# Optimization experiments

Hardware: AMD Instinct MI355X
Metric: run time of the kernel (lower is better)

The kernel has to match this reference:

```python
import jax, jax.numpy as jnp
import numpy as np

IN_DIM, HIDDEN_DIM, OUT_DIM = 128, 256, 128
N_NODES, N_EDGES = 100000, 1000000


def setup_inputs() -> dict:
    key = jax.random.key(0)
    ks = jax.random.split(key, 8)
    s = lambda d: 1.0 / np.sqrt(d)
    x = jax.random.normal(ks[0], (N_NODES, IN_DIM), dtype=jnp.float32)
    edge_index = jax.random.randint(ks[1], (2, N_EDGES), 0, N_NODES, dtype=jnp.int64)
    # encoder: Linear(in,hid) -> ReLU -> Linear(hid,out)
    W1 = jax.random.uniform(ks[2], (IN_DIM, HIDDEN_DIM), jnp.float32, -s(IN_DIM), s(IN_DIM))
    b1 = jnp.zeros((HIDDEN_DIM,), jnp.float32)
    W2 = jax.random.uniform(ks[3], (HIDDEN_DIM, OUT_DIM), jnp.float32, -s(HIDDEN_DIM), s(HIDDEN_DIM))
    b2 = jnp.zeros((OUT_DIM,), jnp.float32)
    # pred: Linear(2*out,hid) -> ReLU -> Linear(hid,1)
    W3 = jax.random.uniform(ks[4], (2 * OUT_DIM, HIDDEN_DIM), jnp.float32, -s(2 * OUT_DIM), s(2 * OUT_DIM))
    b3 = jnp.zeros((HIDDEN_DIM,), jnp.float32)
    W4 = jax.random.uniform(ks[5], (HIDDEN_DIM, 1), jnp.float32, -s(HIDDEN_DIM), s(HIDDEN_DIM))
    b4 = jnp.zeros((1,), jnp.float32)
    return {"x": x, "edge_index": edge_index, "W1": W1, "b1": b1, "W2": W2,
            "b2": b2, "W3": W3, "b3": b3, "W4": W4, "b4": b4}


def reference(x, edge_index, W1, b1, W2, b2, W3, b3, W4, b4):
    # node encoder
    h = jax.nn.relu(x @ W1 + b1) @ W2 + b2            # [N, out_dim]
    # edge gather + concat
    h_src = h[edge_index[0]]                          # [E, out_dim]
    h_dst = h[edge_index[1]]                          # [E, out_dim]
    e = jnp.concatenate([h_src, h_dst], axis=-1)      # [E, 2*out_dim]
    # edge predictor
    logits = jax.nn.relu(e @ W3 + b3) @ W4 + b4       # [E, 1]
    return jax.nn.sigmoid(logits)
```

## Files before the change

kernel.cpp:

```cpp
#include <hip/hip_runtime.h>


#define NN 100000
#define NE 1000000
#define NTN 1563
#define GRID_EP 2048

typedef __attribute__((ext_vector_type(8))) __bf16 bf16x8;
typedef __attribute__((ext_vector_type(4))) float f32x4;
typedef __attribute__((ext_vector_type(4))) unsigned short us4;

__device__ __forceinline__ unsigned short f2bf(float f) {
    unsigned u = __float_as_uint(f);
    return (unsigned short)((u + 0x7FFFu + ((u >> 16) & 1u)) >> 16);
}
__device__ __forceinline__ float bflo(unsigned w) {
    return __uint_as_float(w << 16);
}
__device__ __forceinline__ float bfhi(unsigned w) {
    return __uint_as_float(w & 0xffff0000u);
}

template <int CTRL>
__device__ __forceinline__ float dpp_add(float v) {
    return v + __int_as_float(__builtin_amdgcn_update_dpp(
                   0, __float_as_int(v), CTRL, 0xF, 0xF, true));
}
__device__ __forceinline__ float row_reduce16(float v) {
    v = dpp_add<0x118>(v);
    v = dpp_add<0x114>(v);
    v = dpp_add<0x112>(v);
    v = dpp_add<0x111>(v);
    return v;
}

__global__ void prep1(const float* __restrict__ W1, const float* __restrict__ W2,
                      const float* __restrict__ W3, const float* __restrict__ b2,
                      const float* __restrict__ b3, const float* __restrict__ W4,
                      const void* __restrict__ eidx,
                      unsigned short* __restrict__ w1s,
                      unsigned short* __restrict__ wuts,
                      unsigned short* __restrict__ wvts, float* __restrict__ bu,
                      float* __restrict__ bv, float* __restrict__ w4p,
                      int* __restrict__ flag) {
    int t = blockIdx.x * blockDim.x + threadIdx.x;
    if (t < 32768) {
        int k = t >> 8, n = t & 255;
        w1s[(k >> 3) * 2048 + n * 8 + (k & 7)] = f2bf(W1[t]);
    }
    if (t < 65536) {
        int k = t >> 8, n = t & 255;
        float s = 0.0f;
        for (int j = 0; j < 128; ++j) s += W2[k * 128 + j] * W3[j * 256 + n];
        wuts[(k >> 3) * 2048 + n * 8 + (k & 7)] = f2bf(s);
    } else {
        int i = t - 65536;
        int k = i >> 8, n = i & 255;
        float s = 0.0f;
        for (int j = 0; j < 128; ++j) s += W2[k * 128 + j] * W3[(128 + j) * 256 + n];
        wvts[(k >> 3) * 2048 + n * 8 + (k & 7)] = f2bf(s);
    }
    if (t < 256) {
        float s = b3[t];
        for (int j = 0; j < 128; ++j) s += b2[j] * W3[j * 256 + t];
        bu[t] = s;
    } else if (t < 512) {
        int n = t - 256;
        float s = 0.0f;
        for (int j = 0; j < 128; ++j) s += b2[j] * W3[(128 + j) * 256 + n];
        bv[n] = s;
    } else if (t < 768) {
        int p = t - 512;
        int wq = p >> 6, local = p & 63;
        w4p[p] = W4[wq * 64 + (local & 3) * 16 + ((local >> 2) & 15)];
    }
    if (t == 0) {
        const unsigned* u = (const unsigned*)eidx;
        int all0 = 1;
        for (int i = 0; i < 32; ++i) all0 &= (u[2 * i + 1] == 0u);
        *flag = all0;
    }
}

__global__ __launch_bounds__(256, 3) void node_uv(
    const float* __restrict__ x, const float* __restrict__ b1,
    const unsigned short* __restrict__ w1s, const unsigned short* __restrict__ wuts,
    const unsigned short* __restrict__ wvts, const float* __restrict__ bu,
    const float* __restrict__ bv, unsigned short* __restrict__ Ug,
    unsigned short* __restrict__ Vg) {
    __shared__ __align__(16) unsigned short A1[64 * 136];
    __shared__ __align__(16) unsigned short A2[64 * 264];

    const int t = threadIdx.x, lane = t & 63, w = t >> 6;
    const int cl = lane & 15, q = lane >> 4;
    const int nb = w * 64;
    const int m0 = blockIdx.x * 64;

    {
        const float4* x4 = (const float4*)x;
#pragma unroll
        for (int i = 0; i < 8; ++i) {
            int lin = i * 256 + t;
            int m = lin >> 5, c = lin & 31;
            int node = m0 + m;
            if (node > NN - 1) node = NN - 1;
            float4 v = x4[node * 32 + c];
            us4 b;
            b.x = f2bf(v.x); b.y = f2bf(v.y); b.z = f2bf(v.z); b.w = f2bf(v.w);
            *(us4*)(A1 + m * 136 + c * 4) = b;
        }
    }
    float b1v[4], buv[4], bvv[4];
#pragma unroll
    for (int nt = 0; nt < 4; ++nt) {
        int n = nb + nt * 16 + cl;
        b1v[nt] = b1[n];
        buv[nt] = bu[n];
        bvv[nt] = bv[n];
    }
    __syncthreads();

    {
        f32x4 acc[4][4];
#pragma unroll
        for (int mt = 0; mt < 4; ++mt)
#pragma unroll
            for (int nt = 0; nt < 4; ++nt)
                acc[mt][nt] = (f32x4){b1v[nt], b1v[nt], b1v[nt], b1v[nt]};
#pragma unroll
        for (int s = 0; s < 4; ++s) {
            bf16x8 a[4], bw[4];
#pragma unroll
            for (int mt = 0; mt < 4; ++mt)
                a[mt] = *(const bf16x8*)(A1 + (mt * 16 + cl) * 136 + s * 32 + q * 8);
#pragma unroll
            for (int nt = 0; nt < 4; ++nt)
                bw[nt] = *(const bf16x8*)(w1s + (s * 4 + q) * 2048 +
                                          (nb + nt * 16 + cl) * 8);
#pragma unroll
            for (int mt = 0; mt < 4; ++mt)
#pragma unroll
                for (int nt = 0; nt < 4; ++nt)
                    acc[mt][nt] = __builtin_amdgcn_mfma_f32_16x16x32_bf16(
                        a[mt], bw[nt], acc[mt][nt], 0, 0, 0);
        }
#pragma unroll
        for (int mt = 0; mt < 4; ++mt)
#pragma unroll
            for (int nt = 0; nt < 4; ++nt)
#pragma unroll
                for (int r = 0; r < 4; ++r) {
                    float v = fmaxf(acc[mt][nt][r], 0.0f);
                    A2[(mt * 16 + q * 4 + r) * 264 + nb + nt * 16 + cl] = f2bf(v);
                }
    }
    __syncthreads();

#pragma unroll
    for (int pass = 0; pass < 2; ++pass) {
        const unsigned short* wt = pass ? wvts : wuts;
        unsigned short* outg = pass ? Vg : Ug;
        f32x4 acc[4][4];
#pragma unroll
        for (int mt = 0; mt < 4; ++mt)
#pragma unroll
            for (int nt = 0; nt < 4; ++nt) {
                float bb = pass ? bvv[nt] : buv[nt];
                acc[mt][nt] = (f32x4){bb, bb, bb, bb};
            }
#pragma unroll
        for (int s = 0; s < 8; ++s) {
            bf16x8 a[4], bw[4];
#pragma unroll
            for (int mt = 0; mt < 4; ++mt)
                a[mt] = *(const bf16x8*)(A2 + (mt * 16 + cl) * 264 + s * 32 + q * 8);
#pragma unroll
            for (int nt = 0; nt < 4; ++nt)
                bw[nt] = *(const bf16x8*)(wt + (s * 4 + q) * 2048 +
                                          (nb + nt * 16 + cl) * 8);
#pragma unroll
            for (int mt = 0; mt < 4; ++mt)
#pragma unroll
                for (int nt = 0; nt < 4; ++nt)
                    acc[mt][nt] = __builtin_amdgcn_mfma_f32_16x16x32_bf16(
                        a[mt], bw[nt], acc[mt][nt], 0, 0, 0);
        }
#pragma unroll
        for (int mt = 0; mt < 4; ++mt)
#pragma unroll
            for (int r = 0; r < 4; ++r) {
                int node = m0 + mt * 16 + q * 4 + r;
                if (node < NN) {
                    us4 v = {f2bf(acc[mt][0][r]), f2bf(acc[mt][1][r]),
                             f2bf(acc[mt][2][r]), f2bf(acc[mt][3][r])};
                    *(us4*)(outg + node * 256 + nb + cl * 4) = v;
                }
            }
    }
}

#define TERM(uw, vw, wa, wb)                                     \
    (fmaxf(bflo(uw) + bflo(vw), 0.0f) * (wa) +                   \
     fmaxf(bfhi(uw) + bfhi(vw), 0.0f) * (wb))

__global__ __launch_bounds__(256, 8) void edge_pred(
    const void* __restrict__ eidx, const unsigned short* __restrict__ Ut,
    const unsigned short* __restrict__ Vt, const float* __restrict__ w4p,
    const float* __restrict__ b4, const int* __restrict__ flag,
    float* __restrict__ out) {
    const int t = threadIdx.x, lane = t & 63;
    const int cl = lane & 15, g = lane >> 4;
    const int gwid = (blockIdx.x * 256 + t) >> 6;
    const int nw = (GRID_EP * 256) >> 6;
    const bool i64f = (*flag != 0);
    const int* ei32 = (const int*)eidx;
    const long long* ei64 = (const long long*)eidx;

    float w4a[8], w4b[8];
#pragma unroll
    for (int j = 0; j < 8; ++j) {
        w4a[j] = w4p[cl * 8 + j];
        w4b[j] = w4p[128 + cl * 8 + j];
    }
    const float b4v = b4[0];

    for (int base = gwid * 8; base < NE; base += nw * 8) {
        const int eA = base + g, eB = base + 4 + g;
        int sA = i64f ? (int)ei64[eA] : ei32[eA];
        int dA = i64f ? (int)ei64[NE + eA] : ei32[NE + eA];
        int sB = i64f ? (int)ei64[eB] : ei32[eB];
        int dB = i64f ? (int)ei64[NE + eB] : ei32[NE + eB];
        sA = sA < 0 ? 0 : (sA > NN - 1 ? NN - 1 : sA);
        dA = dA < 0 ? 0 : (dA > NN - 1 ? NN - 1 : dA);
        sB = sB < 0 ? 0 : (sB > NN - 1 ? NN - 1 : sB);
        dB = dB < 0 ? 0 : (dB > NN - 1 ? NN - 1 : dB);

        const uint4* ua = (const uint4*)(Ut + (long)sA * 256) + cl;
        const uint4* va = (const uint4*)(Vt + (long)dA * 256) + cl;
        const uint4* ub = (const uint4*)(Ut + (long)sB * 256) + cl;
        const uint4* vb = (const uint4*)(Vt + (long)dB * 256) + cl;
        uint4 ua0 = ua[0], ua1 = ua[16];
        uint4 va0 = va[0], va1 = va[16];
        uint4 ub0 = ub[0], ub1 = ub[16];
        uint4 vb0 = vb[0], vb1 = vb[16];

        float accA =
            TERM(ua0.x, va0.x, w4a[0], w4a[1]) + TERM(ua0.y, va0.y, w4a[2], w4a[3]) +
            TERM(ua0.z, va0.z, w4a[4], w4a[5]) + TERM(ua0.w, va0.w, w4a[6], w4a[7]) +
            TERM(ua1.x, va1.x, w4b[0], w4b[1]) + TERM(ua1.y, va1.y, w4b[2], w4b[3]) +
            TERM(ua1.z, va1.z, w4b[4], w4b[5]) + TERM(ua1.w, va1.w, w4b[6], w4b[7]);
        float accB =
            TERM(ub0.x, vb0.x, w4a[0], w4a[1]) + TERM(ub0.y, vb0.y, w4a[2], w4a[3]) +
            TERM(ub0.z, vb0.z, w4a[4], w4a[5]) + TERM(ub0.w, vb0.w, w4a[6], w4a[7]) +
            TERM(ub1.x, vb1.x, w4b[0], w4b[1]) + TERM(ub1.y, vb1.y, w4b[2], w4b[3]) +
            TERM(ub1.z, vb1.z, w4b[4], w4b[5]) + TERM(ub1.w, vb1.w, w4b[6], w4b[7]);

        accA = row_reduce16(accA);
        accB = row_reduce16(accB);
        if (cl == 15) {
            out[eA] = 1.0f / (1.0f + __expf(-(accA + b4v)));
            out[eB] = 1.0f / (1.0f + __expf(-(accB + b4v)));
        }
    }
}

extern "C" void kernel_launch(void* const* d_in, const int* in_sizes, int n_in,
                              void* d_out, int out_size, void* d_ws, size_t ws_size,
                              hipStream_t stream) {
    const float* x  = (const float*)d_in[0];
    const void*  ei = d_in[1];
    const float* W1 = (const float*)d_in[2];
    const float* b1 = (const float*)d_in[3];
    const float* W2 = (const float*)d_in[4];
    const float* b2 = (const float*)d_in[5];
    const float* W3 = (const float*)d_in[6];
    const float* b3 = (const float*)d_in[7];
    const float* W4 = (const float*)d_in[8];
    const float* b4 = (const float*)d_in[9];

    char* ws = (char*)d_ws;
    int* flag            = (int*)ws;
    unsigned short* w1s  = (unsigned short*)(ws + 256);
    unsigned short* wuts = (unsigned short*)(ws + 65792);
    unsigned short* wvts = (unsigned short*)(ws + 196864);
    float* bu            = (float*)(ws + 327936);
    float* bv            = (float*)(ws + 328960);
    float* w4p           = (float*)(ws + 329984);
    unsigned short* Ug   = (unsigned short*)(ws + 1048576);
    unsigned short* Vg   = (unsigned short*)(ws + 52248576);

    prep1<<<512, 256, 0, stream>>>(W1, W2, W3, b2, b3, W4, ei, w1s, wuts, wvts,
                                   bu, bv, w4p, flag);
    node_uv<<<NTN, 256, 0, stream>>>(x, b1, w1s, wuts, wvts, bu, bv, Ug, Vg);
    edge_pred<<<GRID_EP, 256, 0, stream>>>(ei, Ug, Vg, w4p, b4, flag, (float*)d_out);
}
```

Before: 295.8 us.

## Software-pipeline edge gathers with double-buffered registers and alias node LDS buffers

The edge predictor loop now uses two register sets, so gathers for the next group of edges are issued before the current group is computed. Edge-index loads and output stores use nontemporal hints, and the grid shrinks to 1280 blocks with occupancy hint 5. The node encoder reuses one shared buffer for both stages, with an added barrier, so LDS per block drops and occupancy 4 becomes possible. The risks are higher register pressure from the double-buffered loads and an extra barrier in the node kernel.

```diff
diff --git a/kernel.cpp b/kernel.cpp
--- a/kernel.cpp
+++ b/kernel.cpp
@@ -4,11 +4,13 @@
 #define NN 100000
 #define NE 1000000
 #define NTN 1563
-#define GRID_EP 2048
+#define GRID_EP 1280
+#define STEP (((GRID_EP * 256) >> 6) * 8)
 
 typedef __attribute__((ext_vector_type(8))) __bf16 bf16x8;
 typedef __attribute__((ext_vector_type(4))) float f32x4;
 typedef __attribute__((ext_vector_type(4))) unsigned short us4;
+typedef __attribute__((ext_vector_type(4))) unsigned int u32x4;
 
 __device__ __forceinline__ unsigned short f2bf(float f) {
     unsigned u = __float_as_uint(f);
@@ -82,14 +84,15 @@
     }
 }
 
-__global__ __launch_bounds__(256, 3) void node_uv(
+__global__ __launch_bounds__(256, 4) void node_uv(
     const float* __restrict__ x, const float* __restrict__ b1,
     const unsigned short* __restrict__ w1s, const unsigned short* __restrict__ wuts,
     const unsigned short* __restrict__ wvts, const float* __restrict__ bu,
     const float* __restrict__ bv, unsigned short* __restrict__ Ug,
     unsigned short* __restrict__ Vg) {
-    __shared__ __align__(16) unsigned short A1[64 * 136];
-    __shared__ __align__(16) unsigned short A2[64 * 264];
+    __shared__ __align__(16) unsigned short SM[64 * 264];
+    unsigned short* const A1 = SM;
+    unsigned short* const A2 = SM;
 
     const int t = threadIdx.x, lane = t & 63, w = t >> 6;
     const int cl = lane & 15, q = lane >> 4;
@@ -97,16 +100,19 @@
     const int m0 = blockIdx.x * 64;
 
     {
-        const float4* x4 = (const float4*)x;
+        const u32x4* x4 = (const u32x4*)x;
 #pragma unroll
         for (int i = 0; i < 8; ++i) {
             int lin = i * 256 + t;
             int m = lin >> 5, c = lin & 31;
             int node = m0 + m;
             if (node > NN - 1) node = NN - 1;
-            float4 v = x4[node * 32 + c];
+            u32x4 v = __builtin_nontemporal_load(x4 + node * 32 + c);
             us4 b;
-            b.x = f2bf(v.x); b.y = f2bf(v.y); b.z = f2bf(v.z); b.w = f2bf(v.w);
+            b.x = f2bf(__uint_as_float(v.x));
+            b.y = f2bf(__uint_as_float(v.y));
+            b.z = f2bf(__uint_as_float(v.z));
+            b.w = f2bf(__uint_as_float(v.w));
             *(us4*)(A1 + m * 136 + c * 4) = b;
         }
     }
@@ -144,6 +150,7 @@
                     acc[mt][nt] = __builtin_amdgcn_mfma_f32_16x16x32_bf16(
                         a[mt], bw[nt], acc[mt][nt], 0, 0, 0);
         }
+        __syncthreads();
 #pragma unroll
         for (int mt = 0; mt < 4; ++mt)
 #pragma unroll
@@ -203,7 +210,66 @@
     (fmaxf(bflo(uw) + bflo(vw), 0.0f) * (wa) +                   \
      fmaxf(bfhi(uw) + bfhi(vw), 0.0f) * (wb))
 
-__global__ __launch_bounds__(256, 8) void edge_pred(
+#define PREF(P, bb)                                                          \
+    {                                                                        \
+        const int eA = (bb) + g, eB = (bb) + 4 + g;                          \
+        int sA, dA, sB, dB;                                                  \
+        if (i64f) {                                                          \
+            sA = (int)__builtin_nontemporal_load(ei64 + eA);                 \
+            dA = (int)__builtin_nontemporal_load(ei64 + NE + eA);            \
+            sB = (int)__builtin_nontemporal_load(ei64 + eB);                 \
+            dB = (int)__builtin_nontemporal_load(ei64 + NE + eB);            \
+        } else {                                                             \
+            sA = __builtin_nontemporal_load(ei32 + eA);                      \
+            dA = __builtin_nontemporal_load(ei32 + NE + eA);                 \
+            sB = __builtin_nontemporal_load(ei32 + eB);                      \
+            dB = __builtin_nontemporal_load(ei32 + NE + eB);                 \
+        }                                                                    \
+        sA = sA < 0 ? 0 : (sA > NN - 1 ? NN - 1 : sA);                       \
+        dA = dA < 0 ? 0 : (dA > NN - 1 ? NN - 1 : dA);                       \
+        sB = sB < 0 ? 0 : (sB > NN - 1 ? NN - 1 : sB);                       \
+        dB = dB < 0 ? 0 : (dB > NN - 1 ? NN - 1 : dB);                       \
+        const uint4* ua = (const uint4*)(Ut + (long)sA * 256) + cl;          \
+        const uint4* va = (const uint4*)(Vt + (long)dA * 256) + cl;          \
+        const uint4* ub = (const uint4*)(Ut + (long)sB * 256) + cl;          \
+        const uint4* vb = (const uint4*)(Vt + (long)dB * 256) + cl;          \
+        P##ua0 = ua[0]; P##ua1 = ua[16];                                     \
+        P##va0 = va[0]; P##va1 = va[16];                                     \
+        P##ub0 = ub[0]; P##ub1 = ub[16];                                     \
+        P##vb0 = vb[0]; P##vb1 = vb[16];                                     \
+    }
+
+#define COMP(P, bb)                                                          \
+    {                                                                        \
+        float accA =                                                         \
+            TERM(P##ua0.x, P##va0.x, w4a[0], w4a[1]) +                       \
+            TERM(P##ua0.y, P##va0.y, w4a[2], w4a[3]) +                       \
+            TERM(P##ua0.z, P##va0.z, w4a[4], w4a[5]) +                       \
+            TERM(P##ua0.w, P##va0.w, w4a[6], w4a[7]) +                       \
+            TERM(P##ua1.x, P##va1.x, w4b[0], w4b[1]) +                       \
+            TERM(P##ua1.y, P##va1.y, w4b[2], w4b[3]) +                       \
+            TERM(P##ua1.z, P##va1.z, w4b[4], w4b[5]) +                       \
+            TERM(P##ua1.w, P##va1.w, w4b[6], w4b[7]);                        \
+        float accB =                                                         \
+            TERM(P##ub0.x, P##vb0.x, w4a[0], w4a[1]) +                       \
+            TERM(P##ub0.y, P##vb0.y, w4a[2], w4a[3]) +                       \
+            TERM(P##ub0.z, P##vb0.z, w4a[4], w4a[5]) +                       \
+            TERM(P##ub0.w, P##vb0.w, w4a[6], w4a[7]) +                       \
+            TERM(P##ub1.x, P##vb1.x, w4b[0], w4b[1]) +                       \
+            TERM(P##ub1.y, P##vb1.y, w4b[2], w4b[3]) +                       \
+            TERM(P##ub1.z, P##vb1.z, w4b[4], w4b[5]) +                       \
+            TERM(P##ub1.w, P##vb1.w, w4b[6], w4b[7]);                        \
+        accA = row_reduce16(accA);                                           \
+        accB = row_reduce16(accB);                                           \
+        if (cl == 15) {                                                      \
+            __builtin_nontemporal_store(                                     \
+                1.0f / (1.0f + __expf(-(accA + b4v))), out + (bb) + g);      \
+            __builtin_nontemporal_store(                                     \
+                1.0f / (1.0f + __expf(-(accB + b4v))), out + (bb) + 4 + g);  \
+        }                                                                    \
+    }
+
+__global__ __launch_bounds__(256, 5) void edge_pred(
     const void* __restrict__ eidx, const unsigned short* __restrict__ Ut,
     const unsigned short* __restrict__ Vt, const float* __restrict__ w4p,
     const float* __restrict__ b4, const int* __restrict__ flag,
@@ -211,7 +277,6 @@
     const int t = threadIdx.x, lane = t & 63;
     const int cl = lane & 15, g = lane >> 4;
     const int gwid = (blockIdx.x * 256 + t) >> 6;
-    const int nw = (GRID_EP * 256) >> 6;
     const bool i64f = (*flag != 0);
     const int* ei32 = (const int*)eidx;
     const long long* ei64 = (const long long*)eidx;
@@ -224,43 +289,21 @@
     }
     const float b4v = b4[0];
 
-    for (int base = gwid * 8; base < NE; base += nw * 8) {
-        const int eA = base + g, eB = base + 4 + g;
-        int sA = i64f ? (int)ei64[eA] : ei32[eA];
-        int dA = i64f ? (int)ei64[NE + eA] : ei32[NE + eA];
-        int sB = i64f ? (int)ei64[eB] : ei32[eB];
-        int dB = i64f ? (int)ei64[NE + eB] : ei32[NE + eB];
-        sA = sA < 0 ? 0 : (sA > NN - 1 ? NN - 1 : sA);
-        dA = dA < 0 ? 0 : (dA > NN - 1 ? NN - 1 : dA);
-        sB = sB < 0 ? 0 : (sB > NN - 1 ? NN - 1 : sB);
-        dB = dB < 0 ? 0 : (dB > NN - 1 ? NN - 1 : dB);
-
-        const uint4* ua = (const uint4*)(Ut + (long)sA * 256) + cl;
-        const uint4* va = (const uint4*)(Vt + (long)dA * 256) + cl;
-        const uint4* ub = (const uint4*)(Ut + (long)sB * 256) + cl;
-        const uint4* vb = (const uint4*)(Vt + (long)dB * 256) + cl;
-        uint4 ua0 = ua[0], ua1 = ua[16];
-        uint4 va0 = va[0], va1 = va[16];
-        uint4 ub0 = ub[0], ub1 = ub[16];
-        uint4 vb0 = vb[0], vb1 = vb[16];
-
-        float accA =
-            TERM(ua0.x, va0.x, w4a[0], w4a[1]) + TERM(ua0.y, va0.y, w4a[2], w4a[3]) +
-            TERM(ua0.z, va0.z, w4a[4], w4a[5]) + TERM(ua0.w, va0.w, w4a[6], w4a[7]) +
-            TERM(ua1.x, va1.x, w4b[0], w4b[1]) + TERM(ua1.y, va1.y, w4b[2], w4b[3]) +
-            TERM(ua1.z, va1.z, w4b[4], w4b[5]) + TERM(ua1.w, va1.w, w4b[6], w4b[7]);
-        float accB =
-            TERM(ub0.x, vb0.x, w4a[0], w4a[1]) + TERM(ub0.y, vb0.y, w4a[2], w4a[3]) +
-            TERM(ub0.z, vb0.z, w4a[4], w4a[5]) + TERM(ub0.w, vb0.w, w4a[6], w4a[7]) +
-            TERM(ub1.x, vb1.x, w4b[0], w4b[1]) + TERM(ub1.y, vb1.y, w4b[2], w4b[3]) +
-            TERM(ub1.z, vb1.z, w4b[4], w4b[5]) + TERM(ub1.w, vb1.w, w4b[6], w4b[7]);
-
-        accA = row_reduce16(accA);
-        accB = row_reduce16(accB);
-        if (cl == 15) {
-            out[eA] = 1.0f / (1.0f + __expf(-(accA + b4v)));
-            out[eB] = 1.0f / (1.0f + __expf(-(accB + b4v)));
-        }
+    uint4 Aua0, Aua1, Ava0, Ava1, Aub0, Aub1, Avb0, Avb1;
+    uint4 Bua0, Bua1, Bva0, Bva1, Bub0, Bub1, Bvb0, Bvb1;
+
+    int base = gwid * 8;
+    PREF(A, base);
+    int base2 = base + STEP;
+    while (true) {
+        if (base2 < NE) PREF(B, base2);
+        COMP(A, base);
+        if (base2 >= NE) break;
+        base = base2 + STEP;
+        if (base < NE) PREF(A, base);
+        COMP(B, base2);
+        if (base >= NE) break;
+        base2 = base + STEP;
     }
 }
 
```

New measurement: 396.4 us. +34.0%, slower.

## Pipeline edge gathers through LDS with async global_load_lds double buffering

Applied to the files above, without the earlier changes.

The edge predictor now gathers the per-node U/V rows asynchronously into a per-wave double-buffered LDS region using global_load_lds. Edge indices are prefetched two iterations ahead, and the wait on the gather is a manual vmcnt count. Each wave now handles 4 edges per iteration instead of 8, with a smaller grid and a lower occupancy bound. The aim is to keep more gather requests in flight and hide random-access latency, at the cost of LDS traffic, inline-asm waitcnt bookkeeping and extra loads on the tail iterations.

```diff
diff --git a/kernel.cpp b/kernel.cpp
--- a/kernel.cpp
+++ b/kernel.cpp
@@ -4,11 +4,15 @@
 #define NN 100000
 #define NE 1000000
 #define NTN 1563
-#define GRID_EP 2048
+#define GRID_EP 1280
+#define NWAVES (GRID_EP * 4)
+#define STEP4 (NWAVES * 4)
+#define NIT (((NE / 4) + NWAVES - 1) / NWAVES)
 
 typedef __attribute__((ext_vector_type(8))) __bf16 bf16x8;
 typedef __attribute__((ext_vector_type(4))) float f32x4;
 typedef __attribute__((ext_vector_type(4))) unsigned short us4;
+typedef __attribute__((ext_vector_type(4))) unsigned int u32x4;
 
 __device__ __forceinline__ unsigned short f2bf(float f) {
     unsigned u = __float_as_uint(f);
@@ -203,15 +207,53 @@
     (fmaxf(bflo(uw) + bflo(vw), 0.0f) * (wa) +                   \
      fmaxf(bfhi(uw) + bfhi(vw), 0.0f) * (wb))
 
-__global__ __launch_bounds__(256, 8) void edge_pred(
+#define EDOT(u0, u1, v0, v1)                                                 \
+    (TERM(u0.x, v0.x, w4a[0], w4a[1]) + TERM(u0.y, v0.y, w4a[2], w4a[3]) +   \
+     TERM(u0.z, v0.z, w4a[4], w4a[5]) + TERM(u0.w, v0.w, w4a[6], w4a[7]) +   \
+     TERM(u1.x, v1.x, w4b[0], w4b[1]) + TERM(u1.y, v1.y, w4b[2], w4b[3]) +   \
+     TERM(u1.z, v1.z, w4b[4], w4b[5]) + TERM(u1.w, v1.w, w4b[6], w4b[7]))
+
+#define LDIDX(e, s, d)                                                       \
+    {                                                                        \
+        int ee = (e);                                                        \
+        if (i64f) {                                                          \
+            s = (int)ei64[ee];                                               \
+            d = (int)ei64[NE + ee];                                          \
+        } else {                                                             \
+            s = ei32[ee];                                                    \
+            d = ei32[NE + ee];                                               \
+        }                                                                    \
+    }
+
+#define GL16(gp, lp)                                                         \
+    __builtin_amdgcn_global_load_lds(                                        \
+        (const __attribute__((address_space(1))) void*)(gp),                 \
+        (__attribute__((address_space(3))) void*)(lp), 16, 0, 0)
+
+#define ISSUE4(slot, si, di)                                                 \
+    {                                                                        \
+        int s_ = (si), d_ = (di);                                            \
+        s_ = s_ < 0 ? 0 : (s_ > NN - 1 ? NN - 1 : s_);                       \
+        d_ = d_ < 0 ? 0 : (d_ > NN - 1 ? NN - 1 : d_);                       \
+        const char* up_ = (const char*)Ut + (long long)s_ * 512 + cl * 16;   \
+        const char* vp_ = (const char*)Vt + (long long)d_ * 512 + cl * 16;   \
+        char* l_ = &smem[w][slot][0];                                        \
+        GL16(up_, l_);                                                       \
+        GL16(up_ + 256, l_ + 1024);                                          \
+        GL16(vp_, l_ + 2048);                                                \
+        GL16(vp_ + 256, l_ + 3072);                                          \
+    }
+
+__global__ __launch_bounds__(256, 5) void edge_pred(
     const void* __restrict__ eidx, const unsigned short* __restrict__ Ut,
     const unsigned short* __restrict__ Vt, const float* __restrict__ w4p,
     const float* __restrict__ b4, const int* __restrict__ flag,
     float* __restrict__ out) {
-    const int t = threadIdx.x, lane = t & 63;
+    __shared__ __align__(1024) char smem[4][2][4096];
+
+    const int t = threadIdx.x, lane = t & 63, w = t >> 6;
     const int cl = lane & 15, g = lane >> 4;
-    const int gwid = (blockIdx.x * 256 + t) >> 6;
-    const int nw = (GRID_EP * 256) >> 6;
+    const int gwid = (blockIdx.x << 2) + w;
     const bool i64f = (*flag != 0);
     const int* ei32 = (const int*)eidx;
     const long long* ei64 = (const long long*)eidx;
@@ -223,45 +265,46 @@
         w4b[j] = w4p[128 + cl * 8 + j];
     }
     const float b4v = b4[0];
-
-    for (int base = gwid * 8; base < NE; base += nw * 8) {
-        const int eA = base + g, eB = base + 4 + g;
-        int sA = i64f ? (int)ei64[eA] : ei32[eA];
-        int dA = i64f ? (int)ei64[NE + eA] : ei32[NE + eA];
-        int sB = i64f ? (int)ei64[eB] : ei32[eB];
-        int dB = i64f ? (int)ei64[NE + eB] : ei32[NE + eB];
-        sA = sA < 0 ? 0 : (sA > NN - 1 ? NN - 1 : sA);
-        dA = dA < 0 ? 0 : (dA > NN - 1 ? NN - 1 : dA);
-        sB = sB < 0 ? 0 : (sB > NN - 1 ? NN - 1 : sB);
-        dB = dB < 0 ? 0 : (dB > NN - 1 ? NN - 1 : dB);
-
-        const uint4* ua = (const uint4*)(Ut + (long)sA * 256) + cl;
-        const uint4* va = (const uint4*)(Vt + (long)dA * 256) + cl;
-        const uint4* ub = (const uint4*)(Ut + (long)sB * 256) + cl;
-        const uint4* vb = (const uint4*)(Vt + (long)dB * 256) + cl;
-        uint4 ua0 = ua[0], ua1 = ua[16];
-        uint4 va0 = va[0], va1 = va[16];
-        uint4 ub0 = ub[0], ub1 = ub[16];
-        uint4 vb0 = vb[0], vb1 = vb[16];
-
-        float accA =
-            TERM(ua0.x, va0.x, w4a[0], w4a[1]) + TERM(ua0.y, va0.y, w4a[2], w4a[3]) +
-            TERM(ua0.z, va0.z, w4a[4], w4a[5]) + TERM(ua0.w, va0.w, w4a[6], w4a[7]) +
-            TERM(ua1.x, va1.x, w4b[0], w4b[1]) + TERM(ua1.y, va1.y, w4b[2], w4b[3]) +
-            TERM(ua1.z, va1.z, w4b[4], w4b[5]) + TERM(ua1.w, va1.w, w4b[6], w4b[7]);
-        float accB =
-            TERM(ub0.x, vb0.x, w4a[0], w4a[1]) + TERM(ub0.y, vb0.y, w4a[2], w4a[3]) +
-            TERM(ub0.z, vb0.z, w4a[4], w4a[5]) + TERM(ub0.w, vb0.w, w4a[6], w4a[7]) +
-            TERM(ub1.x, vb1.x, w4b[0], w4b[1]) + TERM(ub1.y, vb1.y, w4b[2], w4b[3]) +
-            TERM(ub1.z, vb1.z, w4b[4], w4b[5]) + TERM(ub1.w, vb1.w, w4b[6], w4b[7]);
-
-        accA = row_reduce16(accA);
-        accB = row_reduce16(accB);
-        if (cl == 15) {
-            out[eA] = 1.0f / (1.0f + __expf(-(accA + b4v)));
-            out[eB] = 1.0f / (1.0f + __expf(-(accB + b4v)));
-        }
-    }
+    const unsigned smoff = (unsigned)(size_t)(&smem[w][0][0]);
+
+    int b = gwid * 4;
+    int sP, dP;
+    {
+        int s0, d0, s1, d1;
+        LDIDX(b + g, s0, d0);
+        LDIDX(b + STEP4 + g, s1, d1);
+        ISSUE4(0, s0, d0);
+        ISSUE4(1, s1, d1);
+        LDIDX(b + 2 * STEP4 + g, sP, dP);
+    }
+    int cur = 0;
+    for (int it = 0; it < NIT; ++it) {
+        asm volatile("s_waitcnt vmcnt(4)" ::: "memory");
+        __builtin_amdgcn_sched_barrier(0);
+        const unsigned a = smoff + (unsigned)(cur << 12) + (unsigned)(lane * 16);
+        u32x4 u0, u1, v0, v1;
+        asm volatile("ds_read_b128 %0, %1" : "=v"(u0) : "v"(a));
+        asm volatile("ds_read_b128 %0, %1 offset:1024" : "=v"(u1) : "v"(a));
+        asm volatile("ds_read_b128 %0, %1 offset:2048" : "=v"(v0) : "v"(a));
+        asm volatile("ds_read_b128 %0, %1 offset:3072" : "=v"(v1) : "v"(a));
+        asm volatile("s_waitcnt lgkmcnt(0)" ::: "memory");
+        __builtin_amdgcn_sched_barrier(0);
+
+        float acc = EDOT(u0, u1, v0, v1);
+        acc = row_reduce16(acc);
+        if (b < NE && cl == 15)
+            out[b + g] = 1.0f / (1.0f + __expf(-(acc + b4v)));
+
+        int bn = b + 3 * STEP4;
+        int sN, dN;
+        LDIDX((bn < NE ? bn : 0) + g, sN, dN);
+        ISSUE4(cur, sP, dP);
+        sP = sN;
+        dP = dN;
+        cur ^= 1;
+        b += STEP4;
+    }
+    asm volatile("s_waitcnt vmcnt(0)" ::: "memory");
 }
 
 extern "C" void kernel_launch(void* const* d_in, const int* in_sizes, int n_in,
```

New measurement: 299.6 us. No clear change (+1.3%).

## Bucket edges by source-node block and stage U rows in shared memory

Applied to the files above, without the earlier changes.

The node encoder kernel now also bins every edge into a per-64-source-node bucket using atomics, packing src, dst and edge id into a 64-bit record, with an overflow list for full buckets. A new bucketed edge kernel loads the bucket's 64 U rows into LDS once, then gathers only V rows from global memory for each edge. The aim is to roughly halve the random gather traffic. In exchange it adds an atomic binning pass, extra record writes and reads, an unordered scatter of outputs, and a dependence on workspace size, with the old flat kernel kept as a fallback.

```diff
diff --git a/kernel.cpp b/kernel.cpp
--- a/kernel.cpp
+++ b/kernel.cpp
@@ -4,11 +4,15 @@
 #define NN 100000
 #define NE 1000000
 #define NTN 1563
+#define NB 1563
+#define CAP 1024
+#define CAPSH 10
 #define GRID_EP 2048
 
 typedef __attribute__((ext_vector_type(8))) __bf16 bf16x8;
 typedef __attribute__((ext_vector_type(4))) float f32x4;
 typedef __attribute__((ext_vector_type(4))) unsigned short us4;
+typedef __attribute__((ext_vector_type(4))) unsigned int u32x4;
 
 __device__ __forceinline__ unsigned short f2bf(float f) {
     unsigned u = __float_as_uint(f);
@@ -42,7 +46,7 @@
                       unsigned short* __restrict__ wuts,
                       unsigned short* __restrict__ wvts, float* __restrict__ bu,
                       float* __restrict__ bv, float* __restrict__ w4p,
-                      int* __restrict__ flag) {
+                      int* __restrict__ bcnt, int* __restrict__ flag) {
     int t = blockIdx.x * blockDim.x + threadIdx.x;
     if (t < 32768) {
         int k = t >> 8, n = t & 255;
@@ -73,6 +77,8 @@
         int p = t - 512;
         int wq = p >> 6, local = p & 63;
         w4p[p] = W4[wq * 64 + (local & 3) * 16 + ((local >> 2) & 15)];
+    } else if (t < 768 + NB + 1) {
+        bcnt[t - 768] = 0;
     }
     if (t == 0) {
         const unsigned* u = (const unsigned*)eidx;
@@ -87,7 +93,10 @@
     const unsigned short* __restrict__ w1s, const unsigned short* __restrict__ wuts,
     const unsigned short* __restrict__ wvts, const float* __restrict__ bu,
     const float* __restrict__ bv, unsigned short* __restrict__ Ug,
-    unsigned short* __restrict__ Vg) {
+    unsigned short* __restrict__ Vg, const void* __restrict__ eidx,
+    const int* __restrict__ flag, int* __restrict__ bcnt,
+    unsigned long long* __restrict__ brec, unsigned long long* __restrict__ orec,
+    int bin_on) {
     __shared__ __align__(16) unsigned short A1[64 * 136];
     __shared__ __align__(16) unsigned short A2[64 * 264];
 
@@ -95,6 +104,36 @@
     const int cl = lane & 15, q = lane >> 4;
     const int nb = w * 64;
     const int m0 = blockIdx.x * 64;
+
+    if (bin_on) {
+        const bool i64f = (*flag != 0);
+        const int* ei32 = (const int*)eidx;
+        const long long* ei64 = (const long long*)eidx;
+        const int e0 = blockIdx.x * 640;
+        int emax = e0 + 640;
+        if (emax > NE) emax = NE;
+        for (int e = e0 + t; e < emax; e += 256) {
+            int s, d;
+            if (i64f) {
+                s = (int)ei64[e];
+                d = (int)ei64[NE + e];
+            } else {
+                s = ei32[e];
+                d = ei32[NE + e];
+            }
+            s = s < 0 ? 0 : (s > NN - 1 ? NN - 1 : s);
+            d = d < 0 ? 0 : (d > NN - 1 ? NN - 1 : d);
+            int bk = s >> 6;
+            unsigned long long rec = (unsigned long long)(unsigned)s |
+                                     ((unsigned long long)(unsigned)d << 17) |
+                                     ((unsigned long long)(unsigned)e << 34);
+            int pos = atomicAdd(&bcnt[bk], 1);
+            if (pos < CAP)
+                brec[((long long)bk << CAPSH) + pos] = rec;
+            else
+                orec[atomicAdd(&bcnt[NB], 1)] = rec;
+        }
+    }
 
     {
         const float4* x4 = (const float4*)x;
@@ -203,7 +242,89 @@
     (fmaxf(bflo(uw) + bflo(vw), 0.0f) * (wa) +                   \
      fmaxf(bfhi(uw) + bfhi(vw), 0.0f) * (wb))
 
-__global__ __launch_bounds__(256, 8) void edge_pred(
+#define EDOT(u0, u1, v0, v1)                                                 \
+    (TERM(u0.x, v0.x, w4a[0], w4a[1]) + TERM(u0.y, v0.y, w4a[2], w4a[3]) +   \
+     TERM(u0.z, v0.z, w4a[4], w4a[5]) + TERM(u0.w, v0.w, w4a[6], w4a[7]) +   \
+     TERM(u1.x, v1.x, w4b[0], w4b[1]) + TERM(u1.y, v1.y, w4b[2], w4b[3]) +   \
+     TERM(u1.z, v1.z, w4b[4], w4b[5]) + TERM(u1.w, v1.w, w4b[6], w4b[7]))
+
+#define UPITCH 264
+
+__global__ __launch_bounds__(256, 4) void edge_pred_b(
+    const unsigned short* __restrict__ Ut, const unsigned short* __restrict__ Vt,
+    const float* __restrict__ w4p, const float* __restrict__ b4,
+    const int* __restrict__ bcnt, const unsigned long long* __restrict__ brec,
+    const unsigned long long* __restrict__ orec, float* __restrict__ out) {
+    __shared__ __align__(16) unsigned short ubuf[64 * UPITCH];
+
+    const int t = threadIdx.x, lane = t & 63, w = t >> 6;
+    const int cl = lane & 15, g = lane >> 4;
+    const int b = blockIdx.x;
+    const int u0 = b << 6;
+
+    {
+        const uint4* U4 = (const uint4*)Ut;
+#pragma unroll
+        for (int i = 0; i < 8; ++i) {
+            int c = i * 256 + t;
+            int row = c >> 5, col = c & 31;
+            int node = u0 + row;
+            if (node > NN - 1) node = NN - 1;
+            uint4 v = U4[node * 32 + col];
+            *(uint4*)(ubuf + row * UPITCH + col * 8) = v;
+        }
+    }
+    float w4a[8], w4b[8];
+#pragma unroll
+    for (int j = 0; j < 8; ++j) {
+        w4a[j] = w4p[cl * 8 + j];
+        w4b[j] = w4p[128 + cl * 8 + j];
+    }
+    const float b4v = b4[0];
+    __syncthreads();
+
+    int ne = bcnt[b];
+    if (ne > CAP) ne = CAP;
+    const unsigned long long* R = brec + ((long long)b << CAPSH);
+    const int nit = (ne + 15) >> 4;
+    for (int it = 0; it < nit; ++it) {
+        int idx = it * 16 + w * 4 + g;
+        if (idx < ne) {
+            unsigned long long rec = R[idx];
+            int s_loc = ((int)rec & 0x1FFFF) - u0;
+            int d = (int)(rec >> 17) & 0x1FFFF;
+            int eid = (int)(rec >> 34);
+            const uint4* vp = (const uint4*)(Vt + (long long)d * 256) + cl;
+            uint4 vv0 = vp[0], vv1 = vp[16];
+            u32x4 uu0 = *(const u32x4*)(ubuf + s_loc * UPITCH + cl * 8);
+            u32x4 uu1 = *(const u32x4*)(ubuf + s_loc * UPITCH + 128 + cl * 8);
+            float acc = EDOT(uu0, uu1, vv0, vv1);
+            acc = row_reduce16(acc);
+            if (cl == 15)
+                out[eid] = 1.0f / (1.0f + __expf(-(acc + b4v)));
+        }
+    }
+
+    if (b < 256) {
+        int oc = bcnt[NB];
+        for (int i = b * 16 + w * 4 + g; i < oc; i += 256 * 16) {
+            unsigned long long rec = orec[i];
+            int s = (int)rec & 0x1FFFF;
+            int d = (int)(rec >> 17) & 0x1FFFF;
+            int eid = (int)(rec >> 34);
+            const uint4* up = (const uint4*)(Ut + (long long)s * 256) + cl;
+            const uint4* vp = (const uint4*)(Vt + (long long)d * 256) + cl;
+            uint4 uu0 = up[0], uu1 = up[16];
+            uint4 vv0 = vp[0], vv1 = vp[16];
+            float acc = EDOT(uu0, uu1, vv0, vv1);
+            acc = row_reduce16(acc);
+            if (cl == 15)
+                out[eid] = 1.0f / (1.0f + __expf(-(acc + b4v)));
+        }
+    }
+}
+
+__global__ __launch_bounds__(256, 8) void edge_pred_flat(
     const void* __restrict__ eidx, const unsigned short* __restrict__ Ut,
     const unsigned short* __restrict__ Vt, const float* __restrict__ w4p,
     const float* __restrict__ b4, const int* __restrict__ flag,
@@ -244,17 +365,8 @@
         uint4 ub0 = ub[0], ub1 = ub[16];
         uint4 vb0 = vb[0], vb1 = vb[16];
 
-        float accA =
-            TERM(ua0.x, va0.x, w4a[0], w4a[1]) + TERM(ua0.y, va0.y, w4a[2], w4a[3]) +
-            TERM(ua0.z, va0.z, w4a[4], w4a[5]) + TERM(ua0.w, va0.w, w4a[6], w4a[7]) +
-            TERM(ua1.x, va1.x, w4b[0], w4b[1]) + TERM(ua1.y, va1.y, w4b[2], w4b[3]) +
-            TERM(ua1.z, va1.z, w4b[4], w4b[5]) + TERM(ua1.w, va1.w, w4b[6], w4b[7]);
-        float accB =
-            TERM(ub0.x, vb0.x, w4a[0], w4a[1]) + TERM(ub0.y, vb0.y, w4a[2], w4a[3]) +
-            TERM(ub0.z, vb0.z, w4a[4], w4a[5]) + TERM(ub0.w, vb0.w, w4a[6], w4a[7]) +
-            TERM(ub1.x, vb1.x, w4b[0], w4b[1]) + TERM(ub1.y, vb1.y, w4b[2], w4b[3]) +
-            TERM(ub1.z, vb1.z, w4b[4], w4b[5]) + TERM(ub1.w, vb1.w, w4b[6], w4b[7]);
-
+        float accA = EDOT(ua0, ua1, va0, va1);
+        float accB = EDOT(ub0, ub1, vb0, vb1);
         accA = row_reduce16(accA);
         accB = row_reduce16(accB);
         if (cl == 15) {
@@ -286,11 +398,24 @@
     float* bu            = (float*)(ws + 327936);
     float* bv            = (float*)(ws + 328960);
     float* w4p           = (float*)(ws + 329984);
+    int* bcnt            = (int*)(ws + 331008);
     unsigned short* Ug   = (unsigned short*)(ws + 1048576);
     unsigned short* Vg   = (unsigned short*)(ws + 52248576);
+    unsigned long long* brec = (unsigned long long*)(ws + 103448576);
+    unsigned long long* orec = (unsigned long long*)(ws + 116252672);
+
+    const long long NEED = 124252672LL;
+    const int bucketed = ((long long)ws_size >= NEED) ? 1 : 0;
 
     prep1<<<512, 256, 0, stream>>>(W1, W2, W3, b2, b3, W4, ei, w1s, wuts, wvts,
-                                   bu, bv, w4p, flag);
-    node_uv<<<NTN, 256, 0, stream>>>(x, b1, w1s, wuts, wvts, bu, bv, Ug, Vg);
-    edge_pred<<<GRID_EP, 256, 0, stream>>>(ei, Ug, Vg, w4p, b4, flag, (float*)d_out);
-}
+                                   bu, bv, w4p, bcnt, flag);
+    node_uv<<<NTN, 256, 0, stream>>>(x, b1, w1s, wuts, wvts, bu, bv, Ug, Vg,
+                                     ei, flag, bcnt, brec, orec, bucketed);
+    if (bucketed) {
+        edge_pred_b<<<NB, 256, 0, stream>>>(Ug, Vg, w4p, b4, bcnt, brec, orec,
+                                            (float*)d_out);
+    } else {
+        edge_pred_flat<<<GRID_EP, 256, 0, stream>>>(ei, Ug, Vg, w4p, b4, flag,
+                                                    (float*)d_out);
+    }
+}
```

Result: slower. 378.0 us (+27.8%).
